# Kernel optimization log

Measured on AMD Instinct MI355X. Metric: run time of the kernel, lower is better.

## Reference

```python
import jax, jax.numpy as jnp
import numpy as np

# Module hyperparameters (from init_kwargs)
IN_C, OUT_C = 32, 32
D1, D2 = 64, 64
BW1, BW2 = 5, 5


def dst_mat(N):
    """Orthonormal DST-I matrix: symmetric, involutory (M @ M = I).
    Stands in for the repo's matrix-based WSWA / sin_transform pair
    (both are matrix transforms applied along one axis; their inverses
    are the transposed/identical matrices)."""
    n = jnp.arange(1, N + 1, dtype=jnp.float32)
    return jnp.sqrt(2.0 / (N + 1)) * jnp.sin(jnp.pi * n[:, None] * n[None, :] / (N + 1))


def setup_inputs() -> dict:
    key = jax.random.key(0)
    k1, k2 = jax.random.split(key)
    u = jax.random.normal(k1, (8, IN_C, 256, 256), dtype=jnp.float32)
    scale = 2.0 / (IN_C + OUT_C)
    weights = scale * jax.random.uniform(k2, (IN_C * BW1 * BW2, OUT_C, D1 * D2), dtype=jnp.float32)
    return {"u": u, "weights": weights}


def reference(u, weights):
    B, C, Nx, Ny = u.shape
    Mx, My = dst_mat(Nx), dst_mat(Ny)

    # T_pipe: WSWA along dim -1, sin_transform along dim -2 (matrix transforms)
    a = jnp.einsum('bcxy,ym->bcxm', u, My)
    a = jnpum if False else jnp.einsum('bcxy,xm->bcmy', a, Mx)

    # truncate frequency block and unfold (im2col) with kernel (BW1, BW2)
    at = a[..., :D1 + BW1 - 1, :D2 + BW2 - 1]
    # torch.nn.Unfold channel order: c * bw1*bw2 + ki * bw2 + kj
    patches = jnp.stack(
        [at[..., i:i + D1, j:j + D2] for i in range(BW1) for j in range(BW2)],
        axis=2,
    )  # [B, C, BW1*BW2, D1, D2]
    xpad = patches.reshape(B, C * BW1 * BW2, D1 * D2)

    # position-dependent quasi-diagonal batched matmul
    y = jnp.einsum('bix,iox->box', xpad, weights)  # [B, OUT_C, D1*D2]

    # scatter into zero-padded spectral tensor
    b = jnp.zeros((B, OUT_C, Nx, Ny), dtype=u.dtype).at[..., :D1, :D2].set(
        y.reshape(B, OUT_C, D1, D2))

    # iT_pipe: inverse transforms (DST-I is involutory -> same matrices)
    out = jnp.einsum('bcxy,ym->bcxm', b, My)
    out = jnp.einsum('bcxy,xm->bcmy', out, Mx)
    return out
```

## Files before the change

kernel.cpp:

```cpp
#include <hip/hip_runtime.h>
#include <math.h>

#define BCH  8
#define INC  32
#define OUTC 32
#define NSZ  256
#define DD   64
#define BW   5
#define TT   68

__global__ void build_dst(float* __restrict__ Mmat) {
    int idx = blockIdx.x * blockDim.x + threadIdx.x;
    if (idx >= NSZ * NSZ) return;
    int i = idx >> 8, j = idx & 255;
    double arg = M_PI * (double)((i + 1) * (j + 1)) / 257.0;
    Mmat[idx] = (float)(sqrt(2.0 / 257.0) * sin(arg));
}

__global__ __launch_bounds__(256) void gemm_nn(
    const float* __restrict__ A, const float* __restrict__ B, float* __restrict__ C,
    int M, int N, int K, int lda, int ldb, int ldc,
    long long sA, long long sB, long long sC)
{
    const int batch = blockIdx.z;
    A += (long long)batch * sA;
    B += (long long)batch * sB;
    C += (long long)batch * sC;
    const int mt = blockIdx.y * 64;
    const int nt = blockIdx.x * 64;

    __shared__ float As[16][68];
    __shared__ float Bs[16][68];

    const int tid = threadIdx.x;
    const int tx = tid & 15;
    const int ty = tid >> 4;

    const int ar = tid >> 2;
    const int ac = (tid & 3) * 4;
    const int br = tid >> 4;
    const int bc = (tid & 15) * 4;

    float acc[4][4] = {};

    for (int k0 = 0; k0 < K; k0 += 16) {
        float4 av = make_float4(0.f, 0.f, 0.f, 0.f);
        if (mt + ar < M)
            av = *(const float4*)&A[(long long)(mt + ar) * lda + (k0 + ac)];
        As[ac + 0][ar] = av.x;
        As[ac + 1][ar] = av.y;
        As[ac + 2][ar] = av.z;
        As[ac + 3][ar] = av.w;

        if (nt + bc + 3 < N) {
            float4 bv = *(const float4*)&B[(long long)(k0 + br) * ldb + (nt + bc)];
            Bs[br][bc + 0] = bv.x;
            Bs[br][bc + 1] = bv.y;
            Bs[br][bc + 2] = bv.z;
            Bs[br][bc + 3] = bv.w;
        } else {
            #pragma unroll
            for (int t = 0; t < 4; ++t)
                Bs[br][bc + t] = (nt + bc + t < N)
                               ? B[(long long)(k0 + br) * ldb + (nt + bc + t)] : 0.f;
        }
        __syncthreads();

        #pragma unroll
        for (int kk = 0; kk < 16; ++kk) {
            float4 a4 = *(const float4*)&As[kk][ty * 4];
            float4 b4 = *(const float4*)&Bs[kk][tx * 4];
            float a_[4] = {a4.x, a4.y, a4.z, a4.w};
            float b_[4] = {b4.x, b4.y, b4.z, b4.w};
            #pragma unroll
            for (int i = 0; i < 4; ++i)
                #pragma unroll
                for (int j = 0; j < 4; ++j)
                    acc[i][j] += a_[i] * b_[j];
        }
        __syncthreads();
    }

    #pragma unroll
    for (int i = 0; i < 4; ++i) {
        int row = mt + ty * 4 + i;
        if (row < M) {
            #pragma unroll
            for (int j = 0; j < 4; ++j) {
                int col = nt + tx * 4 + j;
                if (col < N)
                    C[(long long)row * ldc + col] = acc[i][j];
            }
        }
    }
}

__global__ __launch_bounds__(256) void spectral_conv(
    const float* __restrict__ at, const float* __restrict__ W, float* __restrict__ y)
{
    const int d1  = blockIdx.x;
    const int og  = blockIdx.y;
    const int tid = threadIdx.x;
    const int d2  = tid & 63;
    const int oty = tid >> 6;
    const int o   = og * 4 + oty;
    const int x   = d1 * 64 + d2;

    __shared__ float ats[BCH][BW][TT];

    float acc[BCH] = {};

    for (int c = 0; c < INC; ++c) {
        __syncthreads();
        for (int idx = tid; idx < BCH * BW * TT; idx += 256) {
            int b = idx / (BW * TT);
            int r = idx % (BW * TT);
            int i = r / TT;
            int q = r % TT;
            ats[b][i][q] = at[((b * INC + c) * TT + (d1 + i)) * TT + q];
        }
        __syncthreads();

        #pragma unroll
        for (int i = 0; i < BW; ++i) {
            #pragma unroll
            for (int j = 0; j < BW; ++j) {
                float w = W[(((c * 25 + i * 5 + j) * OUTC + o) << 12) + x];
                #pragma unroll
                for (int b = 0; b < BCH; ++b)
                    acc[b] += ats[b][i][d2 + j] * w;
            }
        }
    }

    #pragma unroll
    for (int b = 0; b < BCH; ++b)
        y[((b * OUTC + o) << 12) + x] = acc[b];
}

extern "C" void kernel_launch(void* const* d_in, const int* in_sizes, int n_in,
                              void* d_out, int out_size, void* d_ws, size_t ws_size,
                              hipStream_t stream) {
    const float* u = (const float*)d_in[0];
    const float* W = (const float*)d_in[1];
    float* out = (float*)d_out;

    float* ws = (float*)d_ws;
    float* Mm = ws;
    float* t1 = Mm + NSZ * NSZ;
    float* atb = t1 + 256 * (TT * NSZ);
    float* yb  = atb + 256 * (TT * TT);
    float* sb  = t1;

    build_dst<<<dim3((NSZ * NSZ + 255) / 256), dim3(256), 0, stream>>>(Mm);

    gemm_nn<<<dim3(4, 2, 256), dim3(256), 0, stream>>>(
        Mm, u, t1, TT, NSZ, NSZ, NSZ, NSZ, NSZ,
        0LL, (long long)NSZ * NSZ, (long long)TT * NSZ);

    gemm_nn<<<dim3(2, 2, 256), dim3(256), 0, stream>>>(
        t1, Mm, atb, TT, TT, NSZ, NSZ, NSZ, TT,
        (long long)TT * NSZ, 0LL, (long long)TT * TT);

    spectral_conv<<<dim3(64, 8), dim3(256), 0, stream>>>(atb, W, yb);

    gemm_nn<<<dim3(4, 1, 256), dim3(256), 0, stream>>>(
        yb, Mm, sb, DD, NSZ, DD, DD, NSZ, NSZ,
        (long long)DD * DD, 0LL, (long long)DD * NSZ);

    gemm_nn<<<dim3(4, 4, 256), dim3(256), 0, stream>>>(
        Mm, sb, out, NSZ, NSZ, DD, NSZ, NSZ, NSZ,
        0LL, (long long)DD * NSZ, (long long)NSZ * NSZ);
}
```

Measured before the change: 859.1 us.

## Add 128x128 GEMM tiles and split-K spectral conv with vectorized weights

Result: faster. 728.4 us (-15.2%).

```diff
diff --git a/kernel.cpp b/kernel.cpp
--- a/kernel.cpp
+++ b/kernel.cpp
@@ -8,6 +8,8 @@
 #define DD   64
 #define BW   5
 #define TT   68
+#define CCH  8
+#define CPC  4
 
 __global__ void build_dst(float* __restrict__ Mmat) {
     int idx = blockIdx.x * blockDim.x + threadIdx.x;
@@ -35,7 +37,6 @@
     const int tid = threadIdx.x;
     const int tx = tid & 15;
     const int ty = tid >> 4;
-
     const int ar = tid >> 2;
     const int ac = (tid & 3) * 4;
     const int br = tid >> 4;
@@ -95,47 +96,158 @@
     }
 }
 
-__global__ __launch_bounds__(256) void spectral_conv(
-    const float* __restrict__ at, const float* __restrict__ W, float* __restrict__ y)
+__global__ __launch_bounds__(256) void gemm128(
+    const float* __restrict__ A, const float* __restrict__ B, float* __restrict__ C,
+    int Mstore, int K, int lda, int ldb, int ldc,
+    long long sA, long long sB, long long sC)
+{
+    const int batch = blockIdx.z;
+    A += (long long)batch * sA;
+    B += (long long)batch * sB;
+    C += (long long)batch * sC;
+    const int mt = blockIdx.y * 128;
+    const int nt = blockIdx.x * 128;
+
+    __shared__ float As[16][128];
+    __shared__ float Bs[16][128];
+
+    const int tid = threadIdx.x;
+    const int tx = tid & 15;
+    const int ty = tid >> 4;
+    const int n0 = tx * 8;
+    const int m0 = ty * 8;
+
+    float acc[8][8] = {};
+
+    for (int k0 = 0; k0 < K; k0 += 16) {
+        #pragma unroll
+        for (int t = 0; t < 2; ++t) {
+            int idx = tid * 2 + t;
+            int r = idx >> 2;
+            int q = idx & 3;
+            float4 av = *(const float4*)&A[(long long)(mt + r) * lda + (k0 + q * 4)];
+            As[q * 4 + 0][r] = av.x;
+            As[q * 4 + 1][r] = av.y;
+            As[q * 4 + 2][r] = av.z;
+            As[q * 4 + 3][r] = av.w;
+        }
+        #pragma unroll
+        for (int t = 0; t < 2; ++t) {
+            int idx = tid * 2 + t;
+            int r = idx >> 5;
+            int q = idx & 31;
+            float4 bv = *(const float4*)&B[(long long)(k0 + r) * ldb + (nt + q * 4)];
+            *(float4*)&Bs[r][q * 4] = bv;
+        }
+        __syncthreads();
+
+        #pragma unroll
+        for (int kk = 0; kk < 16; ++kk) {
+            float4 a0 = *(const float4*)&As[kk][m0];
+            float4 a1 = *(const float4*)&As[kk][m0 + 4];
+            float4 b0 = *(const float4*)&Bs[kk][n0];
+            float4 b1 = *(const float4*)&Bs[kk][n0 + 4];
+            float a_[8] = {a0.x, a0.y, a0.z, a0.w, a1.x, a1.y, a1.z, a1.w};
+            float b_[8] = {b0.x, b0.y, b0.z, b0.w, b1.x, b1.y, b1.z, b1.w};
+            #pragma unroll
+            for (int i = 0; i < 8; ++i)
+                #pragma unroll
+                for (int j = 0; j < 8; ++j)
+                    acc[i][j] += a_[i] * b_[j];
+        }
+        __syncthreads();
+    }
+
+    #pragma unroll
+    for (int i = 0; i < 8; ++i) {
+        int row = mt + m0 + i;
+        if (row < Mstore) {
+            float4 c0 = make_float4(acc[i][0], acc[i][1], acc[i][2], acc[i][3]);
+            float4 c1 = make_float4(acc[i][4], acc[i][5], acc[i][6], acc[i][7]);
+            *(float4*)&C[(long long)row * ldc + nt + n0]     = c0;
+            *(float4*)&C[(long long)row * ldc + nt + n0 + 4] = c1;
+        }
+    }
+}
+
+__global__ __launch_bounds__(256, 2) void spectral_conv2(
+    const float* __restrict__ at, const float* __restrict__ W, float* __restrict__ yp)
 {
     const int d1  = blockIdx.x;
-    const int og  = blockIdx.y;
+    const int cc  = blockIdx.y;
     const int tid = threadIdx.x;
-    const int d2  = tid & 63;
-    const int oty = tid >> 6;
-    const int o   = og * 4 + oty;
-    const int x   = d1 * 64 + d2;
-
-    __shared__ float ats[BCH][BW][TT];
-
-    float acc[BCH] = {};
-
-    for (int c = 0; c < INC; ++c) {
-        __syncthreads();
-        for (int idx = tid; idx < BCH * BW * TT; idx += 256) {
-            int b = idx / (BW * TT);
-            int r = idx % (BW * TT);
-            int i = r / TT;
-            int q = r % TT;
-            ats[b][i][q] = at[((b * INC + c) * TT + (d1 + i)) * TT + q];
+    const int tx  = tid & 7;
+    const int o   = tid >> 3;
+    const int xb  = d1 * 64 + tx * 8;
+
+    __shared__ float ats[BCH * BW * TT];
+
+    float acc[BCH][8] = {};
+
+    for (int cl = 0; cl < CPC; ++cl) {
+        const int c = cc * CPC + cl;
+        __syncthreads();
+        for (int idx = tid; idx < 680; idx += 256) {
+            int r  = idx / 17;
+            int q4 = idx % 17;
+            int b  = r / 5;
+            int i  = r % 5;
+            float4 v = *(const float4*)&at[(((b * INC + c) * TT) + d1 + i) * TT + q4 * 4];
+            *(float4*)&ats[r * TT + q4 * 4] = v;
         }
         __syncthreads();
 
         #pragma unroll
         for (int i = 0; i < BW; ++i) {
+            float wj[BW][8];
             #pragma unroll
             for (int j = 0; j < BW; ++j) {
-                float w = W[(((c * 25 + i * 5 + j) * OUTC + o) << 12) + x];
+                const float* wp = &W[(((long long)(c * 25 + i * 5 + j) * OUTC + o) << 12) + xb];
+                float4 w0 = *(const float4*)&wp[0];
+                float4 w1 = *(const float4*)&wp[4];
+                wj[j][0] = w0.x; wj[j][1] = w0.y; wj[j][2] = w0.z; wj[j][3] = w0.w;
+                wj[j][4] = w1.x; wj[j][5] = w1.y; wj[j][6] = w1.z; wj[j][7] = w1.w;
+            }
+            #pragma unroll
+            for (int b = 0; b < BCH; ++b) {
+                const float* ar = &ats[(b * BW + i) * TT + tx * 8];
+                float4 a0 = *(const float4*)&ar[0];
+                float4 a1 = *(const float4*)&ar[4];
+                float4 a2 = *(const float4*)&ar[8];
+                float av[12] = {a0.x, a0.y, a0.z, a0.w,
+                                a1.x, a1.y, a1.z, a1.w,
+                                a2.x, a2.y, a2.z, a2.w};
                 #pragma unroll
-                for (int b = 0; b < BCH; ++b)
-                    acc[b] += ats[b][i][d2 + j] * w;
+                for (int j = 0; j < BW; ++j)
+                    #pragma unroll
+                    for (int k = 0; k < 8; ++k)
+                        acc[b][k] += av[j + k] * wj[j][k];
             }
         }
     }
 
-    #pragma unroll
-    for (int b = 0; b < BCH; ++b)
-        y[((b * OUTC + o) << 12) + x] = acc[b];
+    float* yo = yp + (long long)cc * (BCH * OUTC * 4096);
+    #pragma unroll
+    for (int b = 0; b < BCH; ++b) {
+        float4 c0 = make_float4(acc[b][0], acc[b][1], acc[b][2], acc[b][3]);
+        float4 c1 = make_float4(acc[b][4], acc[b][5], acc[b][6], acc[b][7]);
+        float* p = &yo[((b * OUTC + o) << 12) + xb];
+        *(float4*)&p[0] = c0;
+        *(float4*)&p[4] = c1;
+    }
+}
+
+__global__ __launch_bounds__(256) void reduce8(
+    const float* __restrict__ yp, float* __restrict__ yb)
+{
+    int idx = blockIdx.x * blockDim.x + threadIdx.x;
+    float4 s = make_float4(0.f, 0.f, 0.f, 0.f);
+    #pragma unroll
+    for (int p = 0; p < CCH; ++p) {
+        float4 v = *(const float4*)&yp[(long long)p * (BCH * OUTC * 4096) + idx * 4];
+        s.x += v.x; s.y += v.y; s.z += v.z; s.w += v.w;
+    }
+    *(float4*)&yb[idx * 4] = s;
 }
 
 extern "C" void kernel_launch(void* const* d_in, const int* in_sizes, int n_in,
@@ -150,25 +262,27 @@
     float* t1 = Mm + NSZ * NSZ;
     float* atb = t1 + 256 * (TT * NSZ);
     float* yb  = atb + 256 * (TT * TT);
+    float* ypart = yb + BCH * OUTC * 4096;
     float* sb  = t1;
 
     build_dst<<<dim3((NSZ * NSZ + 255) / 256), dim3(256), 0, stream>>>(Mm);
 
-    gemm_nn<<<dim3(4, 2, 256), dim3(256), 0, stream>>>(
-        Mm, u, t1, TT, NSZ, NSZ, NSZ, NSZ, NSZ,
+    gemm128<<<dim3(2, 1, 256), dim3(256), 0, stream>>>(
+        Mm, u, t1, TT, NSZ, NSZ, NSZ, NSZ,
         0LL, (long long)NSZ * NSZ, (long long)TT * NSZ);
 
     gemm_nn<<<dim3(2, 2, 256), dim3(256), 0, stream>>>(
         t1, Mm, atb, TT, TT, NSZ, NSZ, NSZ, TT,
         (long long)TT * NSZ, 0LL, (long long)TT * TT);
 
-    spectral_conv<<<dim3(64, 8), dim3(256), 0, stream>>>(atb, W, yb);
+    spectral_conv2<<<dim3(64, CCH), dim3(256), 0, stream>>>(atb, W, ypart);
+    reduce8<<<dim3(1024), dim3(256), 0, stream>>>(ypart, yb);
 
     gemm_nn<<<dim3(4, 1, 256), dim3(256), 0, stream>>>(
         yb, Mm, sb, DD, NSZ, DD, DD, NSZ, NSZ,
         (long long)DD * DD, 0LL, (long long)DD * NSZ);
 
-    gemm_nn<<<dim3(4, 4, 256), dim3(256), 0, stream>>>(
-        Mm, sb, out, NSZ, NSZ, DD, NSZ, NSZ, NSZ,
+    gemm128<<<dim3(2, 2, 256), dim3(256), 0, stream>>>(
+        Mm, sb, out, NSZ, DD, NSZ, NSZ, NSZ,
         0LL, (long long)DD * NSZ, (long long)NSZ * NSZ);
 }
```
